# Optimization experiments

Hardware: AMD Instinct MI355X
Metric: run time of the kernel (lower is better)

The kernel has to match this reference:

```python
import jax, jax.numpy as jnp
from jax import lax
import numpy as np

C = 56; DI = 112; DS = 16; R = 4; K = 4; NB = 10; UP = 3
B, H, W = 1, 64, 64

def conv2d(x, w, b=None, pad=1, groups=1):
    out = lax.conv_general_dilated(x, w, (1, 1), [(pad, pad), (pad, pad)],
                                   feature_group_count=groups,
                                   dimension_numbers=('NCHW', 'OIHW', 'NCHW'))
    if b is not None:
        out = out + b[None, :, None, None]
    return out

def ln_last(x, w, b, eps=1e-5):
    mu = x.mean(-1, keepdims=True)
    var = ((x - mu) ** 2).mean(-1, keepdims=True)
    return (x - mu) / jnp.sqrt(var + eps) * w + b

def ln_cf(x, w, b, eps=1e-6):
    mu = x.mean(1, keepdims=True)
    var = ((x - mu) ** 2).mean(1, keepdims=True)
    return (x - mu) / jnp.sqrt(var + eps) * w[None, :, None, None] + b[None, :, None, None]

def bsconv(x, pw_w, dw_w, dw_b):
    x = conv2d(x, pw_w, pad=0)
    return conv2d(x, dw_w, dw_b, pad=1, groups=dw_w.shape[0])

def ss2d(x, p):
    # x: (B,H,W,C) -> SS2D (VMamba 4-direction selective scan)
    b, h, w, _ = x.shape
    L = h * w
    xz = x @ p['inproj_w'].T                        # (B,H,W,2*DI)
    xin, z = jnp.split(xz, 2, axis=-1)
    xc = jnp.transpose(xin, (0, 3, 1, 2))           # (B,DI,H,W)
    xc = jax.nn.silu(conv2d(xc, p['conv_w'], p['conv_b'], pad=1, groups=DI))
    xf = xc.reshape(b, DI, L)
    xt = jnp.swapaxes(xc, 2, 3).reshape(b, DI, L)
    x_hwwh = jnp.stack([xf, xt], axis=1)            # (B,2,DI,L)
    xs = jnp.concatenate([x_hwwh, jnp.flip(x_hwwh, -1)], axis=1)  # (B,K,DI,L)
    x_dbl = jnp.einsum('bkdl,kcd->bkcl', xs, p['xproj_w'])
    dts, Bs, Cs = jnp.split(x_dbl, [R, R + DS], axis=2)
    dts = jnp.einsum('bkrl,kdr->bkdl', dts, p['dt_w'])
    A = -jnp.exp(p['Alog'].reshape(K, DI, DS))
    delta = jax.nn.softplus(dts + p['dt_b'][None, :, :, None])    # (B,K,DI,L)

    def step(hst, inp):
        dl, xl, bl, cl = inp
        dA = jnp.exp(dl[..., None] * A[None])       # (B,K,DI,DS)
        hst = dA * hst + (dl * xl)[..., None] * bl[:, :, None, :]
        y = jnp.einsum('bkdn,bkn->bkd', hst, cl)
        return hst, y

    seq = (jnp.transpose(delta, (3, 0, 1, 2)), jnp.transpose(xs, (3, 0, 1, 2)),
           jnp.transpose(Bs, (3, 0, 1, 2)), jnp.transpose(Cs, (3, 0, 1, 2)))
    h0 = jnp.zeros((b, K, DI, DS), x.dtype)
    _, ys = lax.scan(step, h0, seq)                 # (L,B,K,DI)
    out_y = jnp.transpose(ys, (1, 2, 3, 0)) + p['D'].reshape(K, DI)[None, :, :, None] * xs
    inv = jnp.flip(out_y[:, 2:4], -1)
    y1 = out_y[:, 0]
    y2 = inv[:, 0]
    y3 = jnp.swapaxes(inv[:, 1].reshape(b, DI, w, h), 2, 3).reshape(b, DI, L)
    y4 = jnp.swapaxes(out_y[:, 1].reshape(b, DI, w, h), 2, 3).reshape(b, DI, L)
    y = jnp.swapaxes(y1 + y2 + y3 + y4, 1, 2).reshape(b, h, w, DI)
    y = ln_last(y, p['onorm_w'], p['onorm_b'])
    y = y * jax.nn.silu(z)
    return y @ p['outproj_w'].T

def safm(x, mfr_w, mfr_b, aggr_w, aggr_b):
    b, c, h, w = x.shape
    ch = c // 4
    parts = jnp.split(x, 4, axis=1)
    outs = []
    for i in range(4):
        s = parts[i]
        f = 2 ** i
        if i > 0:
            s = s.reshape(b, ch, h // f, f, w // f, f).max(axis=(3, 5))
        s = conv2d(s, mfr_w[i], mfr_b[i], pad=1, groups=ch)
        if i > 0:
            s = jnp.repeat(jnp.repeat(s, f, axis=2), f, axis=3)
        outs.append(s)
    out = conv2d(jnp.concatenate(outs, axis=1), aggr_w, aggr_b, pad=0)
    return jax.nn.gelu(out, approximate=False) * x

def afd(x, p):
    xn = jnp.transpose(x, (0, 2, 3, 1))
    xn = xn + ss2d(ln_last(xn, p['ln1_w'], p['ln1_b']), p)   # VSSBlock residual
    x = jnp.transpose(xn, (0, 3, 1, 2))
    x = x + safm(ln_cf(x, p['norm_w'], p['norm_b']), p['mfr_w'], p['mfr_b'], p['aggr_w'], p['aggr_b'])
    return x, x

def _forward(x, fea_pw_w, fea_dw_w, fea_dw_b,
             blk_ln1_w, blk_ln1_b, blk_inproj_w, blk_conv_w, blk_conv_b,
             blk_xproj_w, blk_dt_w, blk_dt_b, blk_Alog, blk_D,
             blk_onorm_w, blk_onorm_b, blk_outproj_w,
             blk_norm_w, blk_norm_b, blk_mfr_w, blk_mfr_b, blk_aggr_w, blk_aggr_b,
             c1_w, c1_b, norm_w, norm_b, c2_pw_w, c2_dw_w, c2_dw_b, up_w, up_b):
    out_fea = bsconv(x, fea_pw_w, fea_dw_w, fea_dw_b)
    bp = {'ln1_w': blk_ln1_w, 'ln1_b': blk_ln1_b, 'inproj_w': blk_inproj_w,
          'conv_w': blk_conv_w, 'conv_b': blk_conv_b, 'xproj_w': blk_xproj_w,
          'dt_w': blk_dt_w, 'dt_b': blk_dt_b, 'Alog': blk_Alog, 'D': blk_D,
          'onorm_w': blk_onorm_w, 'onorm_b': blk_onorm_b, 'outproj_w': blk_outproj_w,
          'norm_w': blk_norm_w, 'norm_b': blk_norm_b, 'mfr_w': blk_mfr_w,
          'mfr_b': blk_mfr_b, 'aggr_w': blk_aggr_w, 'aggr_b': blk_aggr_b}
    _, outs = lax.scan(afd, out_fea, bp)            # (NB,B,C,H,W) in B1..B10 order
    b, _, h, w = out_fea.shape
    trunk = jnp.transpose(outs, (1, 0, 2, 3, 4)).reshape(b, NB * C, h, w)
    out_B = conv2d(trunk, c1_w, c1_b, pad=0)
    out_B = jax.nn.gelu(ln_cf(out_B, norm_w, norm_b), approximate=False)
    out_lr = bsconv(out_B, c2_pw_w, c2_dw_w, c2_dw_b) + out_fea
    up = conv2d(out_lr, up_w, up_b, pad=1)          # (B, 3*UP*UP, H, W)
    oc = up.shape[1] // (UP * UP)
    ps = up.reshape(b, oc, UP, UP, h, w)
    return jnp.transpose(ps, (0, 1, 4, 2, 5, 3)).reshape(b, oc, h * UP, w * UP)

def setup_inputs():
    key = jax.random.key(0)
    ks = iter(jax.random.split(key, 40))
    rn = lambda shape, s=0.05: jax.random.normal(next(ks), shape, jnp.float32) * s
    ones = lambda shape: jnp.ones(shape, jnp.float32)
    zeros = lambda shape: jnp.zeros(shape, jnp.float32)
    return {
        'x': jax.random.normal(next(ks), (B, 3, H, W), jnp.float32),
        'fea_pw_w': rn((C, 3, 1, 1), 0.3),
        'fea_dw_w': rn((C, 1, 3, 3), 0.3),
        'fea_dw_b': zeros((C,)),
        'blk_ln1_w': ones((NB, C)), 'blk_ln1_b': zeros((NB, C)),
        'blk_inproj_w': rn((NB, 2 * DI, C)),
        'blk_conv_w': rn((NB, DI, 1, 3, 3), 0.2), 'blk_conv_b': zeros((NB, DI)),
        'blk_xproj_w': rn((NB, K, R + 2 * DS, DI)),
        'blk_dt_w': rn((NB, K, DI, R), 0.2),
        'blk_dt_b': jnp.full((NB, K, DI), -4.6, jnp.float32),
        'blk_Alog': jnp.broadcast_to(jnp.log(jnp.arange(1, DS + 1, dtype=jnp.float32)), (NB, K * DI, DS)) + jnp.zeros((NB, K * DI, DS), jnp.float32),
        'blk_D': ones((NB, K * DI)),
        'blk_onorm_w': ones((NB, DI)), 'blk_onorm_b': zeros((NB, DI)),
        'blk_outproj_w': rn((NB, C, DI)),
        'blk_norm_w': ones((NB, C)), 'blk_norm_b': zeros((NB, C)),
        'blk_mfr_w': rn((NB, 4, C // 4, 1, 3, 3), 0.2), 'blk_mfr_b': zeros((NB, 4, C // 4)),
        'blk_aggr_w': rn((NB, C, C, 1, 1)), 'blk_aggr_b': zeros((NB, C)),
        'c1_w': rn((C, NB * C, 1, 1)), 'c1_b': zeros((C,)),
        'norm_w': ones((C,)), 'norm_b': zeros((C,)),
        'c2_pw_w': rn((C, C, 1, 1)), 'c2_dw_w': rn((C, 1, 3, 3), 0.2), 'c2_dw_b': zeros((C,)),
        'up_w': rn((3 * UP * UP, C, 3, 3)), 'up_b': zeros((3 * UP * UP,)),
    }

def reference(x, fea_pw_w, fea_dw_w, fea_dw_b,
              blk_ln1_w, blk_ln1_b, blk_inproj_w, blk_conv_w, blk_conv_b,
              blk_xproj_w, blk_dt_w, blk_dt_b, blk_Alog, blk_D,
              blk_onorm_w, blk_onorm_b, blk_outproj_w,
              blk_norm_w, blk_norm_b, blk_mfr_w, blk_mfr_b, blk_aggr_w, blk_aggr_b,
              c1_w, c1_b, norm_w, norm_b, c2_pw_w, c2_dw_w, c2_dw_b, up_w, up_b):
    return _forward(x, fea_pw_w, fea_dw_w, fea_dw_b,
                    blk_ln1_w, blk_ln1_b, blk_inproj_w, blk_conv_w, blk_conv_b,
                    blk_xproj_w, blk_dt_w, blk_dt_b, blk_Alog, blk_D,
                    blk_onorm_w, blk_onorm_b, blk_outproj_w,
                    blk_norm_w, blk_norm_b, blk_mfr_w, blk_mfr_b, blk_aggr_w, blk_aggr_b,
                    c1_w, c1_b, norm_w, norm_b, c2_pw_w, c2_dw_w, c2_dw_b, up_w, up_b)
```

## Files before the change

### kernel.cpp

```cpp
#include <hip/hip_runtime.h>
#include <hip/hip_bf16.h>

#define HW 64
#define L4 4096
#define CC 56
#define DI 112
#define DSN 16
#define NBLK 10

typedef const float* BP;

__device__ __forceinline__ float bf(BP p, int i) { return p[i]; }
__device__ __forceinline__ float siluf(float x) { return x / (1.f + __expf(-x)); }
__device__ __forceinline__ float geluf(float x) { return 0.5f * x * (1.f + erff(x * 0.70710678f)); }

__global__ void k_fea_pw(BP x, BP w, float* __restrict__ t0) {
    int tid = blockIdx.x * blockDim.x + threadIdx.x;
    if (tid >= CC * L4) return;
    int c = tid >> 12, l = tid & 4095;
    float acc = 0.f;
    for (int i = 0; i < 3; ++i) acc += bf(x, i * L4 + l) * bf(w, c * 3 + i);
    t0[tid] = acc;
}

__global__ void __launch_bounds__(256) k_dw3x3t(
        const float* __restrict__ src, BP w, BP bvec, float* __restrict__ dst,
        int act, const float* __restrict__ addsrc) {
    int c = blockIdx.x >> 4;
    int tile = blockIdx.x & 15;
    int y0 = (tile >> 2) * 16, x0 = (tile & 3) * 16;
    __shared__ float sT[18 * 18];
    const float* sc = src + (size_t)c * L4;
    for (int idx = threadIdx.x; idx < 324; idx += 256) {
        int iy = idx / 18, ix = idx - iy * 18;
        int gy = y0 - 1 + iy, gx = x0 - 1 + ix;
        sT[idx] = (gy >= 0 && gy < 64 && gx >= 0 && gx < 64) ? sc[gy * 64 + gx] : 0.f;
    }
    __syncthreads();
    int py = threadIdx.x >> 4, px = threadIdx.x & 15;
    BP wr = w + c * 9;
    float acc = bvec ? bvec[c] : 0.f;
    #pragma unroll
    for (int ky = 0; ky < 3; ++ky)
        #pragma unroll
        for (int kx = 0; kx < 3; ++kx)
            acc += sT[(py + ky) * 18 + px + kx] * wr[ky * 3 + kx];
    if (act) acc = siluf(acc);
    int l = (y0 + py) * 64 + x0 + px;
    if (addsrc) acc += addsrc[(size_t)c * L4 + l];
    dst[(size_t)c * L4 + l] = acc;
}

__global__ void __launch_bounds__(256) k_ln56g(
        const float* __restrict__ part, BP bias, BP w, BP b, float* __restrict__ dst) {
    int lane = threadIdx.x & 63;
    int cg = threadIdx.x >> 6;
    int l0 = blockIdx.x * 64;
    __shared__ float sS[56 * 64];
    __shared__ float sPa[4][64], sPb[4][64];
    __shared__ float sMu[64], sRs[64];
    float ps = 0.f, ps2 = 0.f;
    for (int c = cg * 14; c < cg * 14 + 14; ++c) {
        float v = bias[c];
        #pragma unroll
        for (int z = 0; z < 5; ++z)
            v += part[(size_t)(z * 56 + c) * L4 + l0 + lane];
        sS[c * 64 + lane] = v; ps += v; ps2 += v * v;
    }
    sPa[cg][lane] = ps; sPb[cg][lane] = ps2;
    __syncthreads();
    if (threadIdx.x < 64) {
        float s = sPa[0][lane] + sPa[1][lane] + sPa[2][lane] + sPa[3][lane];
        float s2 = sPb[0][lane] + sPb[1][lane] + sPb[2][lane] + sPb[3][lane];
        float mu = s / 56.f;
        float var = fmaxf(s2 / 56.f - mu * mu, 0.f);
        sMu[lane] = mu; sRs[lane] = rsqrtf(var + 1e-6f);
    }
    __syncthreads();
    float mu = sMu[lane], rs = sRs[lane];
    for (int c = cg * 14; c < cg * 14 + 14; ++c) {
        float v = (sS[c * 64 + lane] - mu) * rs * w[c] + b[c];
        dst[(size_t)c * L4 + l0 + lane] = geluf(v);
    }
}

__global__ void __launch_bounds__(256) k_gemm(
        const float* __restrict__ src, BP w, BP bvec, const float* __restrict__ addsrc,
        float* __restrict__ dst, int nin, int nout) {
    int lane = threadIdx.x & 63;
    int jg = threadIdx.x >> 6;
    int l0 = blockIdx.x * 64;
    int j0 = blockIdx.y * 16;
    __shared__ __align__(16) float sS[56 * 64];
    __shared__ __align__(16) float sw[16 * 56];
    float acc[4] = {0.f, 0.f, 0.f, 0.f};

    for (int i0 = 0; i0 < nin; i0 += 56) {
        __syncthreads();
        for (int idx = threadIdx.x; idx < 56 * 64; idx += 256) {
            int ii = idx >> 6, px = idx & 63;
            sS[idx] = src[(size_t)(i0 + ii) * L4 + l0 + px];
        }
        for (int idx = threadIdx.x; idx < 16 * 56; idx += 256) {
            int jj = idx / 56, ii = idx - jj * 56;
            int j = j0 + jj;
            sw[idx] = (j < nout) ? w[(size_t)j * nin + i0 + ii] : 0.f;
        }
        __syncthreads();
        #pragma unroll
        for (int ii = 0; ii < 56; ii += 4) {
            float s0 = sS[(ii + 0) * 64 + lane];
            float s1 = sS[(ii + 1) * 64 + lane];
            float s2 = sS[(ii + 2) * 64 + lane];
            float s3 = sS[(ii + 3) * 64 + lane];
            #pragma unroll
            for (int jj = 0; jj < 4; ++jj) {
                const float4 wv = *(const float4*)&sw[(jg * 4 + jj) * 56 + ii];
                acc[jj] += s0 * wv.x + s1 * wv.y + s2 * wv.z + s3 * wv.w;
            }
        }
    }
    int l = l0 + lane;
    #pragma unroll
    for (int jj = 0; jj < 4; ++jj) {
        int j = j0 + jg * 4 + jj;
        if (j >= nout) continue;
        float v = acc[jj];
        if (bvec) v += bf(bvec, j);
        size_t idx = (size_t)j * L4 + l;
        if (addsrc) v += addsrc[idx];
        dst[idx] = v;
    }
}

__global__ void __launch_bounds__(256) k_c1(
        const float* __restrict__ src, BP w, float* __restrict__ part) {
    int lane = threadIdx.x & 63;
    int jg = threadIdx.x >> 6;
    int l0 = blockIdx.x * 64;
    int j0 = blockIdx.y * 16;
    int z = blockIdx.z;
    __shared__ __align__(16) float sS[56 * 64];
    __shared__ __align__(16) float sw[16 * 56];
    float acc[4] = {0.f, 0.f, 0.f, 0.f};

    for (int i0 = z * 112; i0 < z * 112 + 112; i0 += 56) {
        __syncthreads();
        for (int idx = threadIdx.x; idx < 56 * 64; idx += 256) {
            int ii = idx >> 6, px = idx & 63;
            sS[idx] = src[(size_t)(i0 + ii) * L4 + l0 + px];
        }
        for (int idx = threadIdx.x; idx < 16 * 56; idx += 256) {
            int jj = idx / 56, ii = idx - jj * 56;
            int j = j0 + jj;
            sw[idx] = (j < 56) ? w[(size_t)j * 560 + i0 + ii] : 0.f;
        }
        __syncthreads();
        #pragma unroll
        for (int ii = 0; ii < 56; ii += 4) {
            float s0 = sS[(ii + 0) * 64 + lane];
            float s1 = sS[(ii + 1) * 64 + lane];
            float s2 = sS[(ii + 2) * 64 + lane];
            float s3 = sS[(ii + 3) * 64 + lane];
            #pragma unroll
            for (int jj = 0; jj < 4; ++jj) {
                const float4 wv = *(const float4*)&sw[(jg * 4 + jj) * 56 + ii];
                acc[jj] += s0 * wv.x + s1 * wv.y + s2 * wv.z + s3 * wv.w;
            }
        }
    }
    int l = l0 + lane;
    #pragma unroll
    for (int jj = 0; jj < 4; ++jj) {
        int j = j0 + jg * 4 + jj;
        if (j < 56) part[(size_t)(z * 56 + j) * L4 + l] = acc[jj];
    }
}

__global__ void __launch_bounds__(256) k_xproj(
        const float* __restrict__ src, BP w, float* __restrict__ dst) {
    int lane = threadIdx.x & 31;
    int jg = threadIdx.x >> 5;
    int l0 = blockIdx.x * 32;
    int j0 = blockIdx.y * 16;
    __shared__ __align__(16) float sS[112 * 32];
    __shared__ __align__(16) float sw[16 * 112];
    float acc[2] = {0.f, 0.f};

    for (int idx = threadIdx.x; idx < 112 * 32; idx += 256) {
        int ii = idx >> 5, px = idx & 31;
        sS[idx] = src[(size_t)ii * L4 + l0 + px];
    }
    for (int idx = threadIdx.x; idx < 16 * 112; idx += 256) {
        int jj = idx / 112, ii = idx - jj * 112;
        sw[idx] = w[(size_t)(j0 + jj) * 112 + ii];
    }
    __syncthreads();
    #pragma unroll
    for (int ii = 0; ii < 112; ii += 4) {
        float s0 = sS[(ii + 0) * 32 + lane];
        float s1 = sS[(ii + 1) * 32 + lane];
        float s2 = sS[(ii + 2) * 32 + lane];
        float s3 = sS[(ii + 3) * 32 + lane];
        #pragma unroll
        for (int jj = 0; jj < 2; ++jj) {
            const float4 wv = *(const float4*)&sw[(jg * 2 + jj) * 112 + ii];
            acc[jj] += s0 * wv.x + s1 * wv.y + s2 * wv.z + s3 * wv.w;
        }
    }
    __syncthreads();
    #pragma unroll
    for (int jj = 0; jj < 2; ++jj)
        sS[(jg * 2 + jj) * 32 + lane] = acc[jj];
    __syncthreads();
    for (int idx = threadIdx.x; idx < 16 * 32; idx += 256) {
        int cidx = idx & 15, l2 = idx >> 4;
        int j = j0 + cidx;
        int k = j / 36, c = j - k * 36;
        dst[((size_t)k * L4 + l0 + l2) * 36 + c] = sS[cidx * 32 + l2];
    }
}

__global__ void __launch_bounds__(256) k_gemm_ln(
        const float* __restrict__ src, BP lnw, BP lnb, BP w,
        float* __restrict__ dst, int nout) {
    int lane = threadIdx.x & 63;
    int jg = threadIdx.x >> 6;
    int l0 = blockIdx.x * 64;
    int j0 = blockIdx.y * 16;
    __shared__ __align__(16) float sS[56 * 64];
    __shared__ __align__(16) float sw[16 * 56];
    __shared__ float sLw[56], sLb[56];
    float acc[4] = {0.f, 0.f, 0.f, 0.f};

    for (int idx = threadIdx.x; idx < 56 * 64; idx += 256) {
        int ii = idx >> 6, px = idx & 63;
        sS[idx] = src[(size_t)ii * L4 + l0 + px];
    }
    for (int idx = threadIdx.x; idx < 16 * 56; idx += 256) {
        int jj = idx / 56, ii = idx - jj * 56;
        int j = j0 + jj;
        sw[idx] = (j < nout) ? w[(size_t)j * 56 + ii] : 0.f;
    }
    if (threadIdx.x < 56) { sLw[threadIdx.x] = lnw[threadIdx.x]; sLb[threadIdx.x] = lnb[threadIdx.x]; }
    __syncthreads();
    if (threadIdx.x < 64) {
        int px = threadIdx.x;
        float s = 0.f, s2 = 0.f;
        for (int ii = 0; ii < 56; ++ii) { float v = sS[ii * 64 + px]; s += v; s2 += v * v; }
        float mu = s / 56.f;
        float var = fmaxf(s2 / 56.f - mu * mu, 0.f);
        float rstd = rsqrtf(var + 1e-5f);
        for (int ii = 0; ii < 56; ++ii)
            sS[ii * 64 + px] = (sS[ii * 64 + px] - mu) * rstd * sLw[ii] + sLb[ii];
    }
    __syncthreads();
    #pragma unroll
    for (int ii = 0; ii < 56; ii += 4) {
        float s0 = sS[(ii + 0) * 64 + lane];
        float s1 = sS[(ii + 1) * 64 + lane];
        float s2 = sS[(ii + 2) * 64 + lane];
        float s3 = sS[(ii + 3) * 64 + lane];
        #pragma unroll
        for (int jj = 0; jj < 4; ++jj) {
            const float4 wv = *(const float4*)&sw[(jg * 4 + jj) * 56 + ii];
            acc[jj] += s0 * wv.x + s1 * wv.y + s2 * wv.z + s3 * wv.w;
        }
    }
    int l = l0 + lane;
    #pragma unroll
    for (int jj = 0; jj < 4; ++jj) {
        int j = j0 + jg * 4 + jj;
        if (j < nout) dst[(size_t)j * L4 + l] = acc[jj];
    }
}

#define SPAD(p) ((p) + ((p) >> 5))
__global__ void __launch_bounds__(1024, 8) k_scan(
        const float* __restrict__ xc, const float* __restrict__ pk,
        BP Alog, BP dtw, BP dtb, float* __restrict__ ybuf) {
    int pair = blockIdx.x;
    int n = threadIdx.x & 15;
    int c = threadIdx.x >> 4;
    int k = pair / DI, d = pair - k * DI;
    float a = -__expf(Alog[pair * DSN + n]);
    float w0 = dtw[pair * 4 + 0], w1 = dtw[pair * 4 + 1];
    float w2 = dtw[pair * 4 + 2], w3 = dtw[pair * 4 + 3];
    float db = dtb[pair];
    const float* xptr = xc + (size_t)d * L4;
    const float* pkk = pk + (size_t)k * L4 * 36;
    float* yptr = ybuf + (size_t)pair * L4;

    __shared__ float sDl[4224];
    __shared__ float sDlx[4224];
    __shared__ float sP[64 * 16];
    __shared__ float sHe[64 * 16];
    __shared__ float sY[64 * 65];

    for (int p = threadIdx.x; p < L4; p += 1024) {
        const float4 r4 = *(const float4*)(pkk + (size_t)p * 36);
        float v = db + r4.x * w0 + r4.y * w1 + r4.z * w2 + r4.w * w3;
        float dl = fmaxf(v, 0.f) + __logf(1.f + __expf(-fabsf(v)));
        sDl[SPAD(p)] = dl;
        sDlx[SPAD(p)] = dl * xptr[p];
    }
    __syncthreads();

    int p0, dp;
    if (k == 0)      { p0 = c * 64;        dp = 1;   }
    else if (k == 1) { p0 = c;             dp = 64;  }
    else if (k == 2) { p0 = 4095 - c * 64; dp = -1;  }
    else             { p0 = 4095 - c;      dp = -64; }
    long rstep = (long)dp * 36;

    float h = 0.f, P = 1.f;
    {
        int p = p0;
        const float* rB = pkk + (size_t)p0 * 36 + 4 + n;
        for (int jb = 0; jb < 64; jb += 4) {
            float Bv[4], ev[4], dxv[4];
            #pragma unroll
            for (int u = 0; u < 4; ++u) {
                int q = SPAD(p + u * dp);
                Bv[u] = rB[u * rstep];
                ev[u] = __expf(sDl[q] * a);
                dxv[u] = sDlx[q];
            }
            #pragma unroll
            for (int u = 0; u < 4; ++u) {
                h = ev[u] * h + dxv[u] * Bv[u];
                P *= ev[u];
            }
            p += 4 * dp; rB += 4 * rstep;
        }
    }
    int idx = c * 16 + n;
    sP[idx] = P;
    sHe[idx] = h;
    __syncthreads();

    for (int off = 1; off < 64; off <<= 1) {
        float pC = sP[idx], hC = sHe[idx];
        float pL = 0.f, hL = 0.f;
        if (c >= off) { pL = sP[idx - off * 16]; hL = sHe[idx - off * 16]; }
        __syncthreads();
        if (c >= off) { sP[idx] = pC * pL; sHe[idx] = pC * hL + hC; }
        __syncthreads();
    }

    h = (c > 0) ? sHe[idx - 16] : 0.f;
    {
        int p = p0;
        const float* rB = pkk + (size_t)p0 * 36 + 4 + n;
        const float* rC = pkk + (size_t)p0 * 36 + 20 + n;
        for (int jb = 0; jb < 64; jb += 4) {
            float Bv[4], Cv[4], ev[4], dxv[4];
            #pragma unroll
            for (int u = 0; u < 4; ++u) {
                int q = SPAD(p + u * dp);
                Bv[u] = rB[u * rstep];
                Cv[u] = rC[u * rstep];
                ev[u] = __expf(sDl[q] * a);
                dxv[u] = sDlx[q];
            }
            #pragma unroll
            for (int u = 0; u < 4; ++u) {
                h = ev[u] * h + dxv[u] * Bv[u];
                float y = h * Cv[u];
                y += __shfl_xor(y, 1, 16);
                y += __shfl_xor(y, 2, 16);
                y += __shfl_xor(y, 4, 16);
                y += __shfl_xor(y, 8, 16);
                if (n == 0) sY[c * 65 + jb + u] = y;
            }
            p += 4 * dp; rB += 4 * rstep; rC += 4 * rstep;
        }
    }
    __syncthreads();

    for (int pp = threadIdx.x; pp < L4; pp += 1024) {
        int q = (k >= 2) ? (4095 - pp) : pp;
        int cc, jj;
        if (k & 1) { cc = q & 63; jj = q >> 6; }
        else       { cc = q >> 6; jj = q & 63; }
        yptr[pp] = sY[cc * 65 + jj];
    }
}

__global__ void __launch_bounds__(256) k_comb_proj(
        const float* __restrict__ ybuf, const float* __restrict__ xc,
        const float* __restrict__ zbuf, BP Dp, BP ow, BP ob, BP opw,
        const float* __restrict__ xin, BP nw, BP nbv,
        float* __restrict__ x_mid, float* __restrict__ xln) {
    int lane = threadIdx.x & 15;
    int grp = threadIdx.x >> 4;
    int l0 = blockIdx.x * 16;
    __shared__ __align__(16) float sY[112 * 16];
    __shared__ __align__(16) float sW[56 * 112];
    __shared__ float sPa[16][16], sPb[16][16];
    __shared__ float sMu[16], sRs[16];

    float ps = 0.f, ps2 = 0.f;
    for (int d = grp * 7; d < grp * 7 + 7; ++d) {
        float Ds = Dp[d] + Dp[DI + d] + Dp[2 * DI + d] + Dp[3 * DI + d];
        float v = ybuf[(size_t)d * L4 + l0 + lane]
                + ybuf[(size_t)(DI + d) * L4 + l0 + lane]
                + ybuf[(size_t)(2 * DI + d) * L4 + l0 + lane]
                + ybuf[(size_t)(3 * DI + d) * L4 + l0 + lane]
                + Ds * xc[(size_t)d * L4 + l0 + lane];
        sY[d * 16 + lane] = v; ps += v; ps2 += v * v;
    }
    sPa[grp][lane] = ps; sPb[grp][lane] = ps2;
    for (int idx = threadIdx.x; idx < 56 * 112; idx += 256) sW[idx] = opw[idx];
    __syncthreads();
    if (threadIdx.x < 16) {
        float s = 0.f, s2 = 0.f;
        for (int g = 0; g < 16; ++g) { s += sPa[g][lane]; s2 += sPb[g][lane]; }
        float mu = s / 112.f;
        float var = fmaxf(s2 / 112.f - mu * mu, 0.f);
        sMu[lane] = mu; sRs[lane] = rsqrtf(var + 1e-5f);
    }
    __syncthreads();
    {
        float mu = sMu[lane], rs = sRs[lane];
        for (int d = grp * 7; d < grp * 7 + 7; ++d) {
            float v = (sY[d * 16 + lane] - mu) * rs * ow[d] + ob[d];
            float z = zbuf[(size_t)d * L4 + l0 + lane];
            sY[d * 16 + lane] = v * siluf(z);
        }
    }
    __syncthreads();

    float acc[4] = {0.f, 0.f, 0.f, 0.f};
    #pragma unroll 2
    for (int ii = 0; ii < 112; ii += 4) {
        float s0 = sY[(ii + 0) * 16 + lane];
        float s1 = sY[(ii + 1) * 16 + lane];
        float s2 = sY[(ii + 2) * 16 + lane];
        float s3 = sY[(ii + 3) * 16 + lane];
        #pragma unroll
        for (int jj = 0; jj < 4; ++jj) {
            int j = grp * 4 + jj;
            if (j < 56) {
                const float4 wv = *(const float4*)&sW[j * 112 + ii];
                acc[jj] += s0 * wv.x + s1 * wv.y + s2 * wv.z + s3 * wv.w;
            }
        }
    }
    int l = l0 + lane;
    float vout[4];
    float ps3 = 0.f, ps4 = 0.f;
    #pragma unroll
    for (int jj = 0; jj < 4; ++jj) {
        int j = grp * 4 + jj;
        vout[jj] = 0.f;
        if (j < 56) {
            float v = acc[jj] + xin[(size_t)j * L4 + l];
            vout[jj] = v;
            x_mid[(size_t)j * L4 + l] = v;
            ps3 += v; ps4 += v * v;
        }
    }
    __syncthreads();
    sPa[grp][lane] = ps3; sPb[grp][lane] = ps4;
    __syncthreads();
    if (threadIdx.x < 16) {
        float s = 0.f, s2 = 0.f;
        for (int g = 0; g < 16; ++g) { s += sPa[g][lane]; s2 += sPb[g][lane]; }
        float mu = s / 56.f;
        float var = fmaxf(s2 / 56.f - mu * mu, 0.f);
        sMu[lane] = mu; sRs[lane] = rsqrtf(var + 1e-6f);
    }
    __syncthreads();
    {
        float mu = sMu[lane], rs = sRs[lane];
        #pragma unroll
        for (int jj = 0; jj < 4; ++jj) {
            int j = grp * 4 + jj;
            if (j < 56) xln[(size_t)j * L4 + l] = (vout[jj] - mu) * rs * nw[j] + nbv[j];
        }
    }
}

__global__ void __launch_bounds__(256) k_safm(
        const float* __restrict__ xln, BP mw, BP mb,
        float* __restrict__ s0, float* __restrict__ s1,
        float* __restrict__ s2, float* __restrict__ s3) {
    int b = blockIdx.x;
    if (b < 224) {
        int c = b >> 4;
        int tile = b & 15;
        int y0 = (tile >> 2) * 16, x0 = (tile & 3) * 16;
        __shared__ float sT[18 * 18];
        const float* sc = xln + (size_t)c * L4;
        for (int idx = threadIdx.x; idx < 324; idx += 256) {
            int iy = idx / 18, ix = idx - iy * 18;
            int gy = y0 - 1 + iy, gx = x0 - 1 + ix;
            sT[idx] = (gy >= 0 && gy < 64 && gx >= 0 && gx < 64) ? sc[gy * 64 + gx] : 0.f;
        }
        __syncthreads();
        int py = threadIdx.x >> 4, px = threadIdx.x & 15;
        BP wr = mw + c * 9;
        float acc = mb[c];
        #pragma unroll
        for (int ky = 0; ky < 3; ++ky)
            #pragma unroll
            for (int kx = 0; kx < 3; ++kx)
                acc += sT[(py + ky) * 18 + px + kx] * wr[ky * 3 + kx];
        s0[c * L4 + (y0 + py) * 64 + x0 + px] = acc;
    } else {
        int bb = b - 224;
        int i = bb / 14 + 1;
        int c = bb % 14;
        int S = 64 >> i;
        int f = 1 << i;
        __shared__ float sP[34 * 34];
        int W2 = S + 2;
        for (int idx = threadIdx.x; idx < W2 * W2; idx += 256) sP[idx] = 0.f;
        __syncthreads();
        const float* sc = xln + (size_t)(i * 14 + c) * L4;
        for (int cell = threadIdx.x; cell < S * S; cell += 256) {
            int y = cell / S, x = cell - y * S;
            float m = -3.4e38f;
            for (int dy = 0; dy < f; ++dy)
                for (int dx = 0; dx < f; ++dx)
                    m = fmaxf(m, sc[(y * f + dy) * 64 + x * f + dx]);
            sP[(y + 1) * W2 + x + 1] = m;
        }
        __syncthreads();
        BP wr = mw + (i * 14 + c) * 9;
        float bias = mb[i * 14 + c];
        float* dst = (i == 1) ? s1 : (i == 2) ? s2 : s3;
        for (int cell = threadIdx.x; cell < S * S; cell += 256) {
            int y = cell / S, x = cell - y * S;
            float acc = bias;
            #pragma unroll
            for (int ky = 0; ky < 3; ++ky)
                #pragma unroll
                for (int kx = 0; kx < 3; ++kx)
                    acc += sP[(y + ky) * W2 + x + kx] * wr[ky * 3 + kx];
            dst[c * S * S + cell] = acc;
        }
    }
}

__global__ void k_aggr(const float* __restrict__ s0, const float* __restrict__ s1,
                       const float* __restrict__ s2, const float* __restrict__ s3,
                       const float* __restrict__ xln, const float* __restrict__ x_mid,
                       BP aw, BP ab, float* __restrict__ out) {
    int tid = blockIdx.x * blockDim.x + threadIdx.x;
    if (tid >= CC * L4) return;
    int c = tid >> 12, l = tid & 4095;
    int h = l >> 6, w = l & 63;
    int o1 = (h >> 1) * 32 + (w >> 1);
    int o2 = (h >> 2) * 16 + (w >> 2);
    int o3 = (h >> 3) * 8 + (w >> 3);
    float acc = bf(ab, c);
    BP wr = aw + c * 56;
    for (int cg = 0; cg < 14; ++cg) acc += s0[cg * 4096 + l]  * bf(wr, cg);
    for (int cg = 0; cg < 14; ++cg) acc += s1[cg * 1024 + o1] * bf(wr, 14 + cg);
    for (int cg = 0; cg < 14; ++cg) acc += s2[cg * 256 + o2]  * bf(wr, 28 + cg);
    for (int cg = 0; cg < 14; ++cg) acc += s3[cg * 64 + o3]   * bf(wr, 42 + cg);
    out[tid] = x_mid[tid] + geluf(acc) * xln[tid];
}

__global__ void __launch_bounds__(256) k_up(
        const float* __restrict__ out_lr, BP uw, BP ub, float* __restrict__ out) {
    __shared__ float sIn[56 * 36];
    __shared__ float sW[27 * 56 * 9];
    int b = blockIdx.x;
    int y0 = (b >> 4) * 4, x0 = (b & 15) * 4;
    for (int idx = threadIdx.x; idx < 56 * 36; idx += 256) {
        int cc = idx / 36; int rem = idx - cc * 36; int iy = rem / 6, ix = rem - iy * 6;
        int gy = y0 - 1 + iy, gx = x0 - 1 + ix;
        sIn[idx] = (gy >= 0 && gy < 64 && gx >= 0 && gx < 64)
                 ? out_lr[(size_t)cc * L4 + gy * 64 + gx] : 0.f;
    }
    for (int idx = threadIdx.x; idx < 27 * 56 * 9; idx += 256) sW[idx] = uw[idx];
    __syncthreads();
    int px = threadIdx.x & 15;
    int og = threadIdx.x >> 4;
    int dy = px >> 2, dx = px & 3;
    for (int oo = 0; oo < 2; ++oo) {
        int o = og * 2 + oo;
        if (o >= 27) break;
        float acc = ub[o];
        const float* wb = &sW[o * 504];
        for (int cc = 0; cc < 56; ++cc) {
            const float* ib = &sIn[cc * 36 + dy * 6 + dx];
            const float* wc = wb + cc * 9;
            acc += ib[0] * wc[0] + ib[1] * wc[1] + ib[2] * wc[2]
                 + ib[6] * wc[3] + ib[7] * wc[4] + ib[8] * wc[5]
                 + ib[12] * wc[6] + ib[13] * wc[7] + ib[14] * wc[8];
        }
        int h = y0 + dy, wv = x0 + dx;
        int ch = o / 9, rr = (o % 9) / 3, ss = o % 3;
        out[ch * 36864 + (h * 3 + rr) * 192 + (wv * 3 + ss)] = acc;
    }
}

extern "C" void kernel_launch(void* const* d_in, const int* in_sizes, int n_in,
                              void* d_out, int out_size, void* d_ws, size_t ws_size,
                              hipStream_t stream) {
    BP in0  = (BP)d_in[0];
    BP in1  = (BP)d_in[1];
    BP in2  = (BP)d_in[2];
    BP in3  = (BP)d_in[3];
    BP in4  = (BP)d_in[4];
    BP in5  = (BP)d_in[5];
    BP in6  = (BP)d_in[6];
    BP in7  = (BP)d_in[7];
    BP in8  = (BP)d_in[8];
    BP in9  = (BP)d_in[9];
    BP in10 = (BP)d_in[10];
    BP in11 = (BP)d_in[11];
    BP in12 = (BP)d_in[12];
    BP in13 = (BP)d_in[13];
    BP in14 = (BP)d_in[14];
    BP in15 = (BP)d_in[15];
    BP in16 = (BP)d_in[16];
    BP in17 = (BP)d_in[17];
    BP in18 = (BP)d_in[18];
    BP in19 = (BP)d_in[19];
    BP in20 = (BP)d_in[20];
    BP in21 = (BP)d_in[21];
    BP in22 = (BP)d_in[22];
    BP in23 = (BP)d_in[23];
    BP in24 = (BP)d_in[24];
    BP in25 = (BP)d_in[25];
    BP in26 = (BP)d_in[26];
    BP in27 = (BP)d_in[27];
    BP in28 = (BP)d_in[28];
    BP in29 = (BP)d_in[29];
    BP in30 = (BP)d_in[30];
    BP in31 = (BP)d_in[31];

    float* ws = (float*)d_ws;
    float* trunk   = ws; ws += 560 * L4;
    float* out_fea = ws; ws += CC * L4;
    float* t0      = ws; ws += CC * L4;
    float* xz      = ws; ws += 224 * L4;
    float* xc      = ws; ws += DI * L4;
    float* pk      = ws; ws += 4 * 36 * L4;
    float* ybuf    = ws; ws += 4 * DI * L4;
    float* x_mid   = ws; ws += CC * L4;
    float* xln     = ws; ws += CC * L4;
    float* s0      = ws; ws += 14 * 4096;
    float* s1      = ws; ws += 14 * 1024;
    float* s2      = ws; ws += 14 * 256;
    float* s3      = ws; ws += 14 * 64;
    float* part    = ws; ws += 5 * 56 * L4;
    float* gB      = ws; ws += CC * L4;
    float* tbuf    = ws; ws += CC * L4;
    float* out_lr  = ws; ws += CC * L4;

    auto nb256 = [](int n) { return dim3((n + 255) / 256); };
    auto gemm_grid = [](int nout) { return dim3(64, (nout + 15) / 16); };

    k_fea_pw<<<nb256(CC * L4), 256, 0, stream>>>(in0, in1, t0);
    k_dw3x3t<<<dim3(CC * 16), 256, 0, stream>>>(t0, in2, in3, out_fea, 0, nullptr);

    for (int nb = 0; nb < NBLK; ++nb) {
        const float* xin = (nb == 0) ? out_fea : trunk + (size_t)(nb - 1) * CC * L4;
        float* xout = trunk + (size_t)nb * CC * L4;
        BP ln1w = in4 + nb * 56,        ln1b = in5 + nb * 56;
        BP ipw  = in6 + nb * 224 * 56;
        BP cw   = in7 + nb * 112 * 9,   cb   = in8 + nb * 112;
        BP xpw  = in9 + nb * 4 * 36 * 112;
        BP dtw  = in10 + nb * 4 * 112 * 4, dtb = in11 + nb * 448;
        BP alog = in12 + nb * 448 * 16, Dp   = in13 + nb * 448;
        BP onw  = in14 + nb * 112,      onb  = in15 + nb * 112;
        BP opw  = in16 + nb * 56 * 112;
        BP nw   = in17 + nb * 56,       nbv  = in18 + nb * 56;
        BP mw   = in19 + nb * 4 * 14 * 9, mb = in20 + nb * 56;
        BP aw   = in21 + nb * 56 * 56,  ab   = in22 + nb * 56;

        k_gemm_ln<<<gemm_grid(224), 256, 0, stream>>>(xin, ln1w, ln1b, ipw, xz, 224);
        k_dw3x3t<<<dim3(DI * 16), 256, 0, stream>>>(xz, cw, cb, xc, 1, nullptr);
        k_xproj<<<dim3(128, 9), 256, 0, stream>>>(xc, xpw, pk);
        k_scan<<<dim3(4 * DI), 1024, 0, stream>>>(xc, pk, alog, dtw, dtb, ybuf);
        k_comb_proj<<<dim3(256), 256, 0, stream>>>(ybuf, xc, xz + 112 * L4, Dp, onw, onb, opw,
                                                   xin, nw, nbv, x_mid, xln);
        k_safm<<<dim3(266), 256, 0, stream>>>(xln, mw, mb, s0, s1, s2, s3);
        k_aggr<<<nb256(CC * L4), 256, 0, stream>>>(s0, s1, s2, s3, xln, x_mid, aw, ab, xout);
    }

    k_c1<<<dim3(64, 4, 5), 256, 0, stream>>>(trunk, in23, part);
    k_ln56g<<<dim3(64), 256, 0, stream>>>(part, in24, in25, in26, gB);
    k_gemm<<<gemm_grid(56), 256, 0, stream>>>(gB, in27, nullptr, nullptr, tbuf, 56, 56);
    k_dw3x3t<<<dim3(CC * 16), 256, 0, stream>>>(tbuf, in28, in29, out_lr, 0, out_fea);
    k_up<<<dim3(256), 256, 0, stream>>>(out_lr, in30, in31, (float*)d_out);
}
```

Measured before the change: 1.297 ms.

## Give each scan thread four state dims and write outputs directly

The selective scan kernel now runs 256 threads per block, with each thread owning four of the sixteen state dimensions, instead of 1024 threads with one dimension each. B and C are loaded as float4, the delta loads are shared across the four states, and the output reduction shrinks to two shuffles within groups of four lanes. The staging of y through shared memory and the final permuted copy are removed, so y is written straight to global memory in scan order. Exp work per thread goes up fourfold, and the direct global stores for the strided directions are uncoalesced.

```diff
diff --git a/kernel.cpp b/kernel.cpp
--- a/kernel.cpp
+++ b/kernel.cpp
@@ -276,16 +276,16 @@
 }
 
 #define SPAD(p) ((p) + ((p) >> 5))
-__global__ void __launch_bounds__(1024, 8) k_scan(
+__global__ void __launch_bounds__(256) k_scan(
         const float* __restrict__ xc, const float* __restrict__ pk,
         BP Alog, BP dtw, BP dtb, float* __restrict__ ybuf) {
     int pair = blockIdx.x;
-    int n = threadIdx.x & 15;
-    int c = threadIdx.x >> 4;
+    int s = threadIdx.x & 3;
+    int c = threadIdx.x >> 2;
     int k = pair / DI, d = pair - k * DI;
-    float a = -__expf(Alog[pair * DSN + n]);
-    float w0 = dtw[pair * 4 + 0], w1 = dtw[pair * 4 + 1];
-    float w2 = dtw[pair * 4 + 2], w3 = dtw[pair * 4 + 3];
+    const float4 al = *(const float4*)(Alog + pair * DSN + s * 4);
+    float a0 = -__expf(al.x), a1 = -__expf(al.y), a2 = -__expf(al.z), a3 = -__expf(al.w);
+    const float4 wdt = *(const float4*)(dtw + pair * 4);
     float db = dtb[pair];
     const float* xptr = xc + (size_t)d * L4;
     const float* pkk = pk + (size_t)k * L4 * 36;
@@ -295,11 +295,10 @@
     __shared__ float sDlx[4224];
     __shared__ float sP[64 * 16];
     __shared__ float sHe[64 * 16];
-    __shared__ float sY[64 * 65];
-
-    for (int p = threadIdx.x; p < L4; p += 1024) {
+
+    for (int p = threadIdx.x; p < L4; p += 256) {
         const float4 r4 = *(const float4*)(pkk + (size_t)p * 36);
-        float v = db + r4.x * w0 + r4.y * w1 + r4.z * w2 + r4.w * w3;
+        float v = db + r4.x * wdt.x + r4.y * wdt.y + r4.z * wdt.z + r4.w * wdt.w;
         float dl = fmaxf(v, 0.f) + __logf(1.f + __expf(-fabsf(v)));
         sDl[SPAD(p)] = dl;
         sDlx[SPAD(p)] = dl * xptr[p];
@@ -313,77 +312,86 @@
     else             { p0 = 4095 - c;      dp = -64; }
     long rstep = (long)dp * 36;
 
-    float h = 0.f, P = 1.f;
+    float h0 = 0.f, h1 = 0.f, h2 = 0.f, h3 = 0.f;
+    float P0 = 1.f, P1 = 1.f, P2 = 1.f, P3 = 1.f;
     {
         int p = p0;
-        const float* rB = pkk + (size_t)p0 * 36 + 4 + n;
+        const float* rB = pkk + (size_t)p0 * 36 + 4 + s * 4;
         for (int jb = 0; jb < 64; jb += 4) {
-            float Bv[4], ev[4], dxv[4];
+            float4 Bv[4]; float dlv[4], dxv[4];
             #pragma unroll
             for (int u = 0; u < 4; ++u) {
+                Bv[u] = *(const float4*)(rB + u * rstep);
                 int q = SPAD(p + u * dp);
-                Bv[u] = rB[u * rstep];
-                ev[u] = __expf(sDl[q] * a);
-                dxv[u] = sDlx[q];
+                dlv[u] = sDl[q]; dxv[u] = sDlx[q];
             }
             #pragma unroll
             for (int u = 0; u < 4; ++u) {
-                h = ev[u] * h + dxv[u] * Bv[u];
-                P *= ev[u];
+                float e0 = __expf(dlv[u] * a0), e1 = __expf(dlv[u] * a1);
+                float e2 = __expf(dlv[u] * a2), e3 = __expf(dlv[u] * a3);
+                h0 = e0 * h0 + dxv[u] * Bv[u].x; P0 *= e0;
+                h1 = e1 * h1 + dxv[u] * Bv[u].y; P1 *= e1;
+                h2 = e2 * h2 + dxv[u] * Bv[u].z; P2 *= e2;
+                h3 = e3 * h3 + dxv[u] * Bv[u].w; P3 *= e3;
             }
             p += 4 * dp; rB += 4 * rstep;
         }
     }
-    int idx = c * 16 + n;
-    sP[idx] = P;
-    sHe[idx] = h;
+    int base = c * 16 + s * 4;
+    sP[base + 0] = P0; sHe[base + 0] = h0;
+    sP[base + 1] = P1; sHe[base + 1] = h1;
+    sP[base + 2] = P2; sHe[base + 2] = h2;
+    sP[base + 3] = P3; sHe[base + 3] = h3;
     __syncthreads();
 
     for (int off = 1; off < 64; off <<= 1) {
-        float pC = sP[idx], hC = sHe[idx];
-        float pL = 0.f, hL = 0.f;
-        if (c >= off) { pL = sP[idx - off * 16]; hL = sHe[idx - off * 16]; }
-        __syncthreads();
-        if (c >= off) { sP[idx] = pC * pL; sHe[idx] = pC * hL + hC; }
-        __syncthreads();
-    }
-
-    h = (c > 0) ? sHe[idx - 16] : 0.f;
+        float pC[4], hC[4], pL[4] = {0.f,0.f,0.f,0.f}, hL[4] = {0.f,0.f,0.f,0.f};
+        #pragma unroll
+        for (int u = 0; u < 4; ++u) { pC[u] = sP[base + u]; hC[u] = sHe[base + u]; }
+        if (c >= off) {
+            #pragma unroll
+            for (int u = 0; u < 4; ++u) { pL[u] = sP[base - off * 16 + u]; hL[u] = sHe[base - off * 16 + u]; }
+        }
+        __syncthreads();
+        if (c >= off) {
+            #pragma unroll
+            for (int u = 0; u < 4; ++u) { sP[base + u] = pC[u] * pL[u]; sHe[base + u] = pC[u] * hL[u] + hC[u]; }
+        }
+        __syncthreads();
+    }
+
+    if (c > 0) {
+        h0 = sHe[base - 16 + 0]; h1 = sHe[base - 16 + 1];
+        h2 = sHe[base - 16 + 2]; h3 = sHe[base - 16 + 3];
+    } else { h0 = h1 = h2 = h3 = 0.f; }
     {
         int p = p0;
-        const float* rB = pkk + (size_t)p0 * 36 + 4 + n;
-        const float* rC = pkk + (size_t)p0 * 36 + 20 + n;
+        const float* rB = pkk + (size_t)p0 * 36 + 4 + s * 4;
+        const float* rC = pkk + (size_t)p0 * 36 + 20 + s * 4;
         for (int jb = 0; jb < 64; jb += 4) {
-            float Bv[4], Cv[4], ev[4], dxv[4];
+            float4 Bv[4], Cv[4]; float dlv[4], dxv[4];
             #pragma unroll
             for (int u = 0; u < 4; ++u) {
+                Bv[u] = *(const float4*)(rB + u * rstep);
+                Cv[u] = *(const float4*)(rC + u * rstep);
                 int q = SPAD(p + u * dp);
-                Bv[u] = rB[u * rstep];
-                Cv[u] = rC[u * rstep];
-                ev[u] = __expf(sDl[q] * a);
-                dxv[u] = sDlx[q];
+                dlv[u] = sDl[q]; dxv[u] = sDlx[q];
             }
             #pragma unroll
             for (int u = 0; u < 4; ++u) {
-                h = ev[u] * h + dxv[u] * Bv[u];
-                float y = h * Cv[u];
-                y += __shfl_xor(y, 1, 16);
-                y += __shfl_xor(y, 2, 16);
-                y += __shfl_xor(y, 4, 16);
-                y += __shfl_xor(y, 8, 16);
-                if (n == 0) sY[c * 65 + jb + u] = y;
+                float e0 = __expf(dlv[u] * a0), e1 = __expf(dlv[u] * a1);
+                float e2 = __expf(dlv[u] * a2), e3 = __expf(dlv[u] * a3);
+                h0 = e0 * h0 + dxv[u] * Bv[u].x;
+                h1 = e1 * h1 + dxv[u] * Bv[u].y;
+                h2 = e2 * h2 + dxv[u] * Bv[u].z;
+                h3 = e3 * h3 + dxv[u] * Bv[u].w;
+                float y = h0 * Cv[u].x + h1 * Cv[u].y + h2 * Cv[u].z + h3 * Cv[u].w;
+                y += __shfl_xor(y, 1, 4);
+                y += __shfl_xor(y, 2, 4);
+                if (s == 0) yptr[p + u * dp] = y;
             }
             p += 4 * dp; rB += 4 * rstep; rC += 4 * rstep;
         }
-    }
-    __syncthreads();
-
-    for (int pp = threadIdx.x; pp < L4; pp += 1024) {
-        int q = (k >= 2) ? (4095 - pp) : pp;
-        int cc, jj;
-        if (k & 1) { cc = q & 63; jj = q >> 6; }
-        else       { cc = q >> 6; jj = q & 63; }
-        yptr[pp] = sY[cc * 65 + jj];
     }
 }
 
@@ -678,7 +686,7 @@
         k_gemm_ln<<<gemm_grid(224), 256, 0, stream>>>(xin, ln1w, ln1b, ipw, xz, 224);
         k_dw3x3t<<<dim3(DI * 16), 256, 0, stream>>>(xz, cw, cb, xc, 1, nullptr);
         k_xproj<<<dim3(128, 9), 256, 0, stream>>>(xc, xpw, pk);
-        k_scan<<<dim3(4 * DI), 1024, 0, stream>>>(xc, pk, alog, dtw, dtb, ybuf);
+        k_scan<<<dim3(4 * DI), 256, 0, stream>>>(xc, pk, alog, dtw, dtb, ybuf);
         k_comb_proj<<<dim3(256), 256, 0, stream>>>(ybuf, xc, xz + 112 * L4, Dp, onw, onb, opw,
                                                    xin, nw, nbv, x_mid, xln);
         k_safm<<<dim3(266), 256, 0, stream>>>(xln, mw, mb, s0, s1, s2, s3);
```

Result: faster. 1.158 ms (-10.7%).
